# Kernel optimization log

Measured on AMD Instinct MI355X. Metric: run time of the kernel, lower is better.

## Reference

```python
import jax, jax.numpy as jnp
import numpy as np
from jax import lax

B, C, H, W = 2, 256, 128, 128
NC, NP = 80, 9  # num_classes, num_points (3x3 dcn kernel)
PAD = 1


def conv2d(x, w, b=None, pad=1):
    out = lax.conv_general_dilated(x, w, (1, 1), [(pad, pad), (pad, pad)],
                                   dimension_numbers=('NCHW', 'OIHW', 'NCHW'))
    if b is not None:
        out = out + b[None, :, None, None]
    return out


def bilinear_sample(img_bhwc, py, px):
    # zero-padded bilinear sampling; py/px: [B,H,W] float coords
    Hi, Wi = img_bhwc.shape[1], img_bhwc.shape[2]
    y0 = jnp.floor(py)
    x0 = jnp.floor(px)
    wy1 = py - y0
    wx1 = px - x0

    def gather(yc, xc, w):
        valid = (yc >= 0) & (yc <= Hi - 1) & (xc >= 0) & (xc <= Wi - 1)
        yi = jnp.clip(yc, 0, Hi - 1).astype(jnp.int32)
        xi = jnp.clip(xc, 0, Wi - 1).astype(jnp.int32)
        v = jax.vmap(lambda im, yy, xx: im[yy, xx])(img_bhwc, yi, xi)  # [B,H,W,C]
        return v * (w * valid)[..., None]

    return (gather(y0, x0, (1 - wy1) * (1 - wx1)) + gather(y0, x0 + 1, (1 - wy1) * wx1)
            + gather(y0 + 1, x0, wy1 * (1 - wx1)) + gather(y0 + 1, x0 + 1, wy1 * wx1))


def deform_conv(x, offset, weight, mask=None, pad=1):
    # x: [B,C,H,W]; offset: [B,2K,H,W] interleaved (dy,dx) per kernel point;
    # mask: [B,K,H,W] or None (modulated DCN multiplies sampled value by mask as-is)
    kh, kw = weight.shape[2], weight.shape[3]
    xb = jnp.transpose(x, (0, 2, 3, 1))  # [B,H,W,C]
    gy, gx = jnp.meshgrid(jnp.arange(x.shape[2], dtype=x.dtype),
                          jnp.arange(x.shape[3], dtype=x.dtype), indexing='ij')
    acc = 0.
    for k in range(kh * kw):  # fixed structural loop over 9 kernel points
        ky, kx = k // kw, k % kw
        py = gy[None] + (ky - pad) + offset[:, 2 * k]
        px = gx[None] + (kx - pad) + offset[:, 2 * k + 1]
        val = bilinear_sample(xb, py, px)  # [B,H,W,C]
        if mask is not None:
            val = val * mask[:, k][..., None]
        acc = acc + jnp.einsum('bhwc,oc->bohw', val, weight[:, :, ky, kx])
    return acc


def setup_inputs() -> dict:
    key = jax.random.key(0)
    ks = jax.random.split(key, 16)
    d = {"x": jax.random.normal(ks[0], (B, C, H, W), jnp.float32)}

    def w(k, shape):
        return jax.random.normal(k, shape, jnp.float32) * 0.01

    i = 1
    for j in range(3):
        d[f"cls_w{j}"] = w(ks[i], (C, C, 3, 3)); i += 1
        d[f"cls_b{j}"] = jnp.zeros((C,), jnp.float32)
        d[f"reg_w{j}"] = w(ks[i], (C, C, 3, 3)); i += 1
        d[f"reg_b{j}"] = jnp.zeros((C,), jnp.float32)
    d["init_conv_w"] = w(ks[i], (C, C, 3, 3)); i += 1
    d["init_conv_b"] = jnp.zeros((C,), jnp.float32)
    d["init_out_w"] = w(ks[i], (3 * NP, C, 1, 1)); i += 1
    d["init_out_b"] = jnp.zeros((3 * NP,), jnp.float32)
    d["dcn_cls_w"] = w(ks[i], (C, C, 3, 3)); i += 1  # ModulatedDeformConv (bias=False)
    d["cls_out_w"] = w(ks[i], (NC, C, 1, 1)); i += 1
    d["cls_out_b"] = jnp.full((NC,), -4.59511985013459, jnp.float32)  # bias_init_with_prob(0.01)
    d["dcn_ref_w"] = w(ks[i], (C, C, 3, 3)); i += 1  # DeformConv (bias=False)
    d["ref_out_w"] = w(ks[i], (2 * NP, C, 1, 1)); i += 1
    d["ref_out_b"] = jnp.zeros((2 * NP,), jnp.float32)
    return d


def reference(x, cls_w0, cls_b0, reg_w0, reg_b0, cls_w1, cls_b1, reg_w1, reg_b1,
              cls_w2, cls_b2, reg_w2, reg_b2, init_conv_w, init_conv_b,
              init_out_w, init_out_b, dcn_cls_w, cls_out_w, cls_out_b,
              dcn_ref_w, ref_out_w, ref_out_b):
    relu = jax.nn.relu
    cls_feat = x
    for wgt, b in ((cls_w0, cls_b0), (cls_w1, cls_b1), (cls_w2, cls_b2)):
        cls_feat = relu(conv2d(cls_feat, wgt, b, 1))
    pts_feat = x
    for wgt, b in ((reg_w0, reg_b0), (reg_w1, reg_b1), (reg_w2, reg_b2)):
        pts_feat = relu(conv2d(pts_feat, wgt, b, 1))

    pts_out_init = conv2d(relu(conv2d(pts_feat, init_conv_w, init_conv_b, 1)),
                          init_out_w, init_out_b, 0)  # [B,27,H,W]
    o1, o2, mask = (pts_out_init[:, :NP], pts_out_init[:, NP:2 * NP],
                    pts_out_init[:, 2 * NP:])
    offset = jnp.concatenate([o1, o2], axis=1)  # dcn_offset (points_init = 0)

    cls_out = conv2d(relu(deform_conv(cls_feat, offset, dcn_cls_w, mask)),
                     cls_out_w, cls_out_b, 0)
    pts_out_refine = conv2d(relu(deform_conv(pts_feat, offset, dcn_ref_w)),
                            ref_out_w, ref_out_b, 0)
    pts_out_refine = pts_out_refine + lax.stop_gradient(offset)

    # pts2wh_offsets
    pts = pts_out_refine.reshape(B, NP, 2, H, W)
    pts_mean = pts.mean(axis=1, keepdims=True)          # [B,1,2,H,W]
    wh = jnp.abs(pts + pts_mean).max(axis=1)            # [B,2,H,W]
    reg = pts_mean[:, 0]                                # [B,2,H,W]
    return (cls_out, wh, reg)
```

## Files before the change

kernel.cpp:

```cpp
#include <hip/hip_runtime.h>

#define Bn 2
#define Cn 256
#define Hn 128
#define Wn 128
#define HWn 16384
#define NCn 80

typedef __attribute__((ext_vector_type(4))) float f32x4;
typedef __attribute__((ext_vector_type(8))) short bf16x8;

__device__ __forceinline__ float blo(unsigned u) {
    union { unsigned u; float f; } x; x.u = u << 16; return x.f;
}
__device__ __forceinline__ float bhi(unsigned u) {
    union { unsigned u; float f; } x; x.u = u & 0xffff0000u; return x.f;
}
__device__ __forceinline__ unsigned short f2bf(float f) {
    union { float f; unsigned u; } x; x.f = f;
    unsigned u = x.u + 0x7fffu + ((x.u >> 16) & 1u);
    return (unsigned short)(u >> 16);
}

#define GLOAD16(gp, lp) __builtin_amdgcn_global_load_lds( \
    (__attribute__((address_space(1))) unsigned int*)(gp), \
    (__attribute__((address_space(3))) unsigned int*)(lp), 16, 0, 0)

__global__ void zeroK(unsigned short* z) { z[threadIdx.x] = 0; }

__global__ __launch_bounds__(256) void xinK(const float* __restrict__ x,
                                            unsigned short* __restrict__ o) {
    __shared__ float tb[32][33];
    const int b = blockIdx.z;
    const int hw0 = blockIdx.x * 32, c0 = blockIdx.y * 32;
    const int tx = threadIdx.x & 31, ty = threadIdx.x >> 5;
    const float* ip = x + ((size_t)(b * Cn + c0)) * HWn + hw0;
#pragma unroll
    for (int r = 0; r < 4; ++r) tb[ty + 8 * r][tx] = ip[(size_t)(ty + 8 * r) * HWn + tx];
    __syncthreads();
    unsigned short* op = o + ((size_t)(b * HWn + hw0)) * Cn + c0;
#pragma unroll
    for (int r = 0; r < 4; ++r) op[(size_t)(ty + 8 * r) * Cn + tx] = f2bf(tb[tx][ty + 8 * r]);
}

struct WPtrs { const float* p[9]; };
__global__ __launch_bounds__(256) void repackAll(WPtrs wsrc, unsigned short* __restrict__ dst) {
    const int t = blockIdx.x * 256 + threadIdx.x;
    const int widx = t >> 16;
    const int r = t & 65535;
    const float* s = wsrc.p[widx] + (size_t)r * 9;
    float v[9];
#pragma unroll
    for (int k = 0; k < 9; ++k) v[k] = s[k];
    unsigned short* d = dst + (size_t)widx * 589824 + r;
#pragma unroll
    for (int k = 0; k < 9; ++k) d[(size_t)k * 65536] = f2bf(v[k]);
}

struct HPtrs { const float* w[3]; };
__global__ __launch_bounds__(256) void repackHeads(HPtrs hs, unsigned short* __restrict__ dst) {
    const int t = blockIdx.x * 256 + threadIdx.x;
    const int ic = t & 255, row = t >> 8;
    int which, oc, OC;
    if (row < 32)       { which = 0; oc = row;       OC = 27; }
    else if (row < 128) { which = 1; oc = row - 32;  OC = 80; }
    else                { which = 2; oc = row - 128; OC = 18; }
    dst[t] = (oc < OC) ? f2bf(hs.w[which][(size_t)oc * Cn + ic]) : (unsigned short)0;
}

struct CJobs {
    const unsigned short* feat[2];
    const unsigned short* W[2];
    const float* bias[2];
    unsigned short* out[2];
};
__global__ __launch_bounds__(256, 2) void convGemm(CJobs jobs,
                                                   const unsigned short* __restrict__ zb) {
    const int jz = blockIdx.z;
    const unsigned short* feat = jobs.feat[jz];
    const unsigned short* Wp = jobs.W[jz];
    const float* bias = jobs.bias[jz];
    unsigned short* outp = jobs.out[jz];

    __shared__ __align__(16) unsigned short lA[2][8192];
    __shared__ __align__(16) unsigned short lB[2][8192];
    const int tid = threadIdx.x;
    const int l = tid & 63, w = tid >> 6;
    const int w_oc = w & 1, w_px = w >> 1;
    const int ry = (blockIdx.x & 7) * 32 + (blockIdx.x >> 3);
    const int b = ry >> 7, y = ry & 127;
    const int oc0 = blockIdx.y * 128;
    const int lr = l & 15, lg = l >> 4;

    int rI[4], cI[4], dI[4];
#pragma unroll
    for (int i = 0; i < 4; ++i) {
        int ps = (i * 4 + w) * 64 + l;
        rI[i] = ps >> 3;
        cI[i] = ((ps & 7) ^ (rI[i] & 7)) * 8;
        dI[i] = (i * 4 + w) * 512;
    }

    f32x4 acc[4][4];
#pragma unroll
    for (int i = 0; i < 4; ++i)
#pragma unroll
        for (int j = 0; j < 4; ++j) acc[i][j] = (f32x4){0.f, 0.f, 0.f, 0.f};

    auto stage = [&](int p, int bufIdx) {
        const int k = p >> 2, c0 = (p & 3) * 64;
        const int dy = k / 3 - 1, dx = k % 3 - 1;
        const int yy = y + dy;
        const bool vy = (unsigned)yy < (unsigned)Hn;
        const size_t fbase = ((size_t)(b * Hn + yy)) * Wn;
        const unsigned short* wk = Wp + (size_t)k * 65536 + (size_t)oc0 * Cn + c0;
        unsigned short* la = lA[bufIdx];
        unsigned short* lb = lB[bufIdx];
#pragma unroll
        for (int i = 0; i < 4; ++i)
            GLOAD16(wk + rI[i] * Cn + cI[i], la + dI[i]);
#pragma unroll
        for (int i = 0; i < 4; ++i) {
            const int pxs = rI[i] + dx;
            const unsigned short* g = (vy && (unsigned)pxs < (unsigned)Wn)
                ? feat + ((fbase + pxs) * Cn + c0 + cI[i])
                : zb;
            GLOAD16(g, lb + dI[i]);
        }
    };

    stage(0, 0);
    __syncthreads();

#pragma unroll 1
    for (int p = 0; p < 36; ++p) {
        const int cur = p & 1;
        if (p < 35) stage(p + 1, cur ^ 1);
        const unsigned short* la = lA[cur];
        const unsigned short* lb = lB[cur];
#pragma unroll
        for (int h = 0; h < 2; ++h) {
            const int ch = h * 4 + lg;
            bf16x8 av[4], bv[4];
#pragma unroll
            for (int fm = 0; fm < 4; ++fm) {
                const int row = w_oc * 64 + fm * 16 + lr;
                av[fm] = *(const bf16x8*)&la[row * 64 + ((ch ^ (row & 7)) * 8)];
            }
#pragma unroll
            for (int fn = 0; fn < 4; ++fn) {
                const int row = w_px * 64 + fn * 16 + lr;
                bv[fn] = *(const bf16x8*)&lb[row * 64 + ((ch ^ (row & 7)) * 8)];
            }
#pragma unroll
            for (int fm = 0; fm < 4; ++fm)
#pragma unroll
                for (int fn = 0; fn < 4; ++fn)
                    acc[fm][fn] = __builtin_amdgcn_mfma_f32_16x16x32_bf16(
                        av[fm], bv[fn], acc[fm][fn], 0, 0, 0);
        }
        __syncthreads();
    }

#pragma unroll
    for (int fm = 0; fm < 4; ++fm) {
        const int ocb = oc0 + w_oc * 64 + fm * 16 + lg * 4;
        const float b0 = bias[ocb], b1 = bias[ocb + 1], b2 = bias[ocb + 2], b3 = bias[ocb + 3];
#pragma unroll
        for (int fn = 0; fn < 4; ++fn) {
            const int px = w_px * 64 + fn * 16 + lr;
            f32x4 v = acc[fm][fn];
            unsigned u0 = (unsigned)f2bf(fmaxf(v[0] + b0, 0.f)) | ((unsigned)f2bf(fmaxf(v[1] + b1, 0.f)) << 16);
            unsigned u1 = (unsigned)f2bf(fmaxf(v[2] + b2, 0.f)) | ((unsigned)f2bf(fmaxf(v[3] + b3, 0.f)) << 16);
            uint2 st; st.x = u0; st.y = u1;
            *(uint2*)&outp[((size_t)ry * Wn + px) * Cn + ocb] = st;
        }
    }
}

template <bool HASMASK>
__global__ __launch_bounds__(512, 4) void dcnGemm(const unsigned short* __restrict__ feat,
                                                  const float* __restrict__ o27,
                                                  const unsigned short* __restrict__ Wp,
                                                  unsigned short* __restrict__ out) {
    __shared__ __align__(16) unsigned short lA[2][16384];
    __shared__ __align__(16) unsigned short lB[2][4096];
    const int tid = threadIdx.x;
    const int l = tid & 63, w = tid >> 6;
    const int w_oc = w & 3, w_px = w >> 2;
    const int g = (blockIdx.x & 7) * 64 + (blockIdx.x >> 3);
    const int ry = g >> 1, st = g & 1;
    const int b = ry >> 7, y = ry & 127;
    const int x0 = st * 64;
    const int lr = l & 15, lg = l >> 4;

    int rIA[4], cIA[4], dIA[4];
#pragma unroll
    for (int i = 0; i < 4; ++i) {
        int ps = (i * 8 + w) * 64 + l;
        rIA[i] = ps >> 3;
        cIA[i] = ((ps & 7) ^ (rIA[i] & 7)) * 8;
        dIA[i] = (i * 8 + w) * 512;
    }

    const int sp = tid >> 3;
    const int pc = tid & 7;
    const int xg = x0 + sp;
    const int wslot = sp * 64 + ((pc ^ (sp & 7)) * 8);

    const float* ob = o27 + (size_t)b * 27 * HWn + y * Wn + xg;
    const unsigned short* fb = feat + (size_t)b * HWn * Cn;

    f32x4 acc[4][2];
#pragma unroll
    for (int i = 0; i < 4; ++i)
#pragma unroll
        for (int j = 0; j < 2; ++j) acc[i][j] = (f32x4){0.f, 0.f, 0.f, 0.f};

    int ci0, ci1, ci2, ci3;
    float cw0, cw1, cw2, cw3;

    auto sampParams = [&](int k) {
        const float offy = ob[(size_t)(2 * k) * HWn];
        const float offx = ob[(size_t)(2 * k + 1) * HWn];
        const float m = HASMASK ? ob[(size_t)(18 + k) * HWn] : 1.f;
        const float py = (float)(y + k / 3 - 1) + offy;
        const float px = (float)(xg + k % 3 - 1) + offx;
        const float y0f = floorf(py), x0f = floorf(px);
        const float wy1 = py - y0f, wx1 = px - x0f;
        const int iy0 = (int)y0f, ix0 = (int)x0f;
        const int iy1 = iy0 + 1, ix1 = ix0 + 1;
        const bool vy0 = (unsigned)iy0 < (unsigned)Hn, vy1 = (unsigned)iy1 < (unsigned)Hn;
        const bool vx0 = (unsigned)ix0 < (unsigned)Wn, vx1 = (unsigned)ix1 < (unsigned)Wn;
        const int yc0 = min(max(iy0, 0), Hn - 1), yc1 = min(max(iy1, 0), Hn - 1);
        const int xc0 = min(max(ix0, 0), Wn - 1), xc1 = min(max(ix1, 0), Wn - 1);
        cw0 = (vy0 && vx0) ? (1.f - wy1) * (1.f - wx1) * m : 0.f;
        cw1 = (vy0 && vx1) ? (1.f - wy1) * wx1 * m : 0.f;
        cw2 = (vy1 && vx0) ? wy1 * (1.f - wx1) * m : 0.f;
        cw3 = (vy1 && vx1) ? wy1 * wx1 * m : 0.f;
        ci0 = (yc0 * Wn + xc0) * Cn;
        ci1 = (yc0 * Wn + xc1) * Cn;
        ci2 = (yc1 * Wn + xc0) * Cn;
        ci3 = (yc1 * Wn + xc1) * Cn;
    };

    int4 q0, q1, q2, q3;
    auto cornerLoads = [&](int p) {
        const int cb = (p & 3) * 64 + pc * 8;
        q0 = *(const int4*)(fb + ci0 + cb);
        q1 = *(const int4*)(fb + ci1 + cb);
        q2 = *(const int4*)(fb + ci2 + cb);
        q3 = *(const int4*)(fb + ci3 + cb);
    };
    auto stageA = [&](int p, int bufIdx) {
        const int k = p >> 2, c0 = (p & 3) * 64;
        const unsigned short* wk = Wp + (size_t)k * 65536 + c0;
        unsigned short* la = lA[bufIdx];
#pragma unroll
        for (int i = 0; i < 4; ++i)
            GLOAD16(wk + rIA[i] * Cn + cIA[i], la + dIA[i]);
    };
    auto interpWrite = [&](int bufIdx) {
        unsigned u[4];
#pragma unroll
        for (int jj = 0; jj < 4; ++jj) {
            const unsigned a0 = ((const unsigned*)&q0)[jj];
            const unsigned a1 = ((const unsigned*)&q1)[jj];
            const unsigned a2 = ((const unsigned*)&q2)[jj];
            const unsigned a3 = ((const unsigned*)&q3)[jj];
            float e0 = cw0 * blo(a0) + cw1 * blo(a1) + cw2 * blo(a2) + cw3 * blo(a3);
            float e1 = cw0 * bhi(a0) + cw1 * bhi(a1) + cw2 * bhi(a2) + cw3 * bhi(a3);
            u[jj] = (unsigned)f2bf(e0) | ((unsigned)f2bf(e1) << 16);
        }
        int4 pk; pk.x = u[0]; pk.y = u[1]; pk.z = u[2]; pk.w = u[3];
        *(int4*)&lB[bufIdx][wslot] = pk;
    };

    sampParams(0);
    stageA(0, 0);
    cornerLoads(0);
    interpWrite(0);
    __syncthreads();

#pragma unroll 1
    for (int p = 0; p < 36; ++p) {
        const int cur = p & 1;
        if (p < 35) {
            if (((p + 1) & 3) == 0) sampParams((p + 1) >> 2);
            stageA(p + 1, cur ^ 1);
            cornerLoads(p + 1);
        }
        const unsigned short* la = lA[cur];
        const unsigned short* lb = lB[cur];
#pragma unroll
        for (int h = 0; h < 2; ++h) {
            const int ch = h * 4 + lg;
            bf16x8 av[4], bv[2];
#pragma unroll
            for (int fm = 0; fm < 4; ++fm) {
                const int row = w_oc * 64 + fm * 16 + lr;
                av[fm] = *(const bf16x8*)&la[row * 64 + ((ch ^ (row & 7)) * 8)];
            }
#pragma unroll
            for (int fn = 0; fn < 2; ++fn) {
                const int row = w_px * 32 + fn * 16 + lr;
                bv[fn] = *(const bf16x8*)&lb[row * 64 + ((ch ^ (row & 7)) * 8)];
            }
#pragma unroll
            for (int fm = 0; fm < 4; ++fm)
#pragma unroll
                for (int fn = 0; fn < 2; ++fn)
                    acc[fm][fn] = __builtin_amdgcn_mfma_f32_16x16x32_bf16(
                        av[fm], bv[fn], acc[fm][fn], 0, 0, 0);
        }
        if (p < 35) interpWrite(cur ^ 1);
        __syncthreads();
    }

#pragma unroll
    for (int fm = 0; fm < 4; ++fm) {
        const int ocb = w_oc * 64 + fm * 16 + lg * 4;
#pragma unroll
        for (int fn = 0; fn < 2; ++fn) {
            const int px = x0 + w_px * 32 + fn * 16 + lr;
            f32x4 v = acc[fm][fn];
            unsigned u0 = (unsigned)f2bf(fmaxf(v[0], 0.f)) | ((unsigned)f2bf(fmaxf(v[1], 0.f)) << 16);
            unsigned u1 = (unsigned)f2bf(fmaxf(v[2], 0.f)) | ((unsigned)f2bf(fmaxf(v[3], 0.f)) << 16);
            uint2 stv; stv.x = u0; stv.y = u1;
            *(uint2*)&out[((size_t)ry * Wn + px) * Cn + ocb] = stv;
        }
    }
}

template <int OC, int PM, bool ADD, bool POST>
__global__ __launch_bounds__(256, 2) void headGemm(const unsigned short* __restrict__ feat,
                                                   const unsigned short* __restrict__ Wp,
                                                   const float* __restrict__ bias,
                                                   float* __restrict__ out,
                                                   const float* __restrict__ add,
                                                   int addC,
                                                   float* __restrict__ reg) {
    constexpr int MF = PM / 16;
    constexpr int NA = PM * 8 / 256;
    __shared__ __align__(16) unsigned short lA[PM * 64];
    __shared__ __align__(16) unsigned short lB[128 * 64];
    __shared__ float lR[POST ? 18 : 1][POST ? 128 : 1];
    const int tid = threadIdx.x;
    const int l = tid & 63, w = tid >> 6;
    const int ry = (blockIdx.x & 7) * 32 + (blockIdx.x >> 3);
    const int b = ry >> 7, y = ry & 127;
    const int lr = l & 15, lg = l >> 4;

    int rIA[NA], cIA[NA], dIA[NA];
#pragma unroll
    for (int i = 0; i < NA; ++i) {
        int ps = (i * 4 + w) * 64 + l;
        rIA[i] = ps >> 3;
        cIA[i] = ((ps & 7) ^ (rIA[i] & 7)) * 8;
        dIA[i] = (i * 4 + w) * 512;
    }
    int rIB[4], cIB[4], dIB[4];
#pragma unroll
    for (int i = 0; i < 4; ++i) {
        int ps = (i * 4 + w) * 64 + l;
        rIB[i] = ps >> 3;
        cIB[i] = ((ps & 7) ^ (rIB[i] & 7)) * 8;
        dIB[i] = (i * 4 + w) * 512;
    }

    f32x4 acc[MF][2];
#pragma unroll
    for (int i = 0; i < MF; ++i)
#pragma unroll
        for (int j = 0; j < 2; ++j) acc[i][j] = (f32x4){0.f, 0.f, 0.f, 0.f};

    const unsigned short* frow = feat + ((size_t)ry * Wn) * Cn;

#pragma unroll 1
    for (int cc = 0; cc < 4; ++cc) {
        const int c0 = cc * 64;
#pragma unroll
        for (int i = 0; i < NA; ++i)
            GLOAD16(Wp + (size_t)rIA[i] * Cn + c0 + cIA[i], &lA[dIA[i]]);
#pragma unroll
        for (int i = 0; i < 4; ++i)
            GLOAD16(frow + (size_t)rIB[i] * Cn + c0 + cIB[i], &lB[dIB[i]]);
        __syncthreads();
#pragma unroll
        for (int h = 0; h < 2; ++h) {
            const int ch = h * 4 + lg;
            bf16x8 av[MF], bv[2];
#pragma unroll
            for (int fm = 0; fm < MF; ++fm) {
                const int row = fm * 16 + lr;
                av[fm] = *(const bf16x8*)&lA[row * 64 + ((ch ^ (row & 7)) * 8)];
            }
#pragma unroll
            for (int fn = 0; fn < 2; ++fn) {
                const int row = w * 32 + fn * 16 + lr;
                bv[fn] = *(const bf16x8*)&lB[row * 64 + ((ch ^ (row & 7)) * 8)];
            }
#pragma unroll
            for (int fm = 0; fm < MF; ++fm)
#pragma unroll
                for (int fn = 0; fn < 2; ++fn)
                    acc[fm][fn] = __builtin_amdgcn_mfma_f32_16x16x32_bf16(
                        av[fm], bv[fn], acc[fm][fn], 0, 0, 0);
        }
        __syncthreads();
    }

    if (!POST) {
#pragma unroll
        for (int fm = 0; fm < MF; ++fm) {
            const int ocb = fm * 16 + lg * 4;
            if (ocb >= OC) break;
#pragma unroll
            for (int j = 0; j < 4; ++j) {
                const int oc = ocb + j;
                if (oc >= OC) break;
                const float bs = bias[oc];
#pragma unroll
                for (int fn = 0; fn < 2; ++fn) {
                    const int px = w * 32 + fn * 16 + lr;
                    float r = acc[fm][fn][j] + bs;
                    if (ADD) r += add[((size_t)(b * addC + oc)) * HWn + y * Wn + px];
                    out[((size_t)(b * OC + oc)) * HWn + y * Wn + px] = r;
                }
            }
        }
    } else {
#pragma unroll
        for (int fm = 0; fm < MF; ++fm) {
            const int ocb = fm * 16 + lg * 4;
#pragma unroll
            for (int j = 0; j < 4; ++j) {
                const int oc = ocb + j;
                if (oc < 18) {
                    const float bs = bias[oc];
#pragma unroll
                    for (int fn = 0; fn < 2; ++fn) {
                        const int px = w * 32 + fn * 16 + lr;
                        float r = acc[fm][fn][j] + bs
                                + add[((size_t)(b * addC + oc)) * HWn + y * Wn + px];
                        lR[oc][px] = r;
                    }
                }
            }
        }
        __syncthreads();
        if (tid < 128) {
            const int px = tid;
            float v[18];
#pragma unroll
            for (int c = 0; c < 18; ++c) v[c] = lR[c][px];
            float s0 = 0.f, s1 = 0.f;
#pragma unroll
            for (int q = 0; q < 9; ++q) { s0 += v[2 * q]; s1 += v[2 * q + 1]; }
            float m0 = s0 * (1.f / 9.f), m1 = s1 * (1.f / 9.f);
            float w0 = 0.f, w1 = 0.f;
#pragma unroll
            for (int q = 0; q < 9; ++q) {
                w0 = fmaxf(w0, fabsf(v[2 * q] + m0));
                w1 = fmaxf(w1, fabsf(v[2 * q + 1] + m1));
            }
            const size_t hw = (size_t)y * Wn + px;
            out[(size_t)(b * 2 + 0) * HWn + hw] = w0;
            out[(size_t)(b * 2 + 1) * HWn + hw] = w1;
            reg[(size_t)(b * 2 + 0) * HWn + hw] = m0;
            reg[(size_t)(b * 2 + 1) * HWn + hw] = m1;
        }
    }
}

extern "C" void kernel_launch(void* const* d_in, const int* in_sizes, int n_in,
                              void* d_out, int out_size, void* d_ws, size_t ws_size,
                              hipStream_t stream) {
    const float* x           = (const float*)d_in[0];
    const float* cls_w0      = (const float*)d_in[1];
    const float* cls_b0      = (const float*)d_in[2];
    const float* reg_w0      = (const float*)d_in[3];
    const float* reg_b0      = (const float*)d_in[4];
    const float* cls_w1      = (const float*)d_in[5];
    const float* cls_b1      = (const float*)d_in[6];
    const float* reg_w1      = (const float*)d_in[7];
    const float* reg_b1      = (const float*)d_in[8];
    const float* cls_w2      = (const float*)d_in[9];
    const float* cls_b2      = (const float*)d_in[10];
    const float* reg_w2      = (const float*)d_in[11];
    const float* reg_b2      = (const float*)d_in[12];
    const float* init_conv_w = (const float*)d_in[13];
    const float* init_conv_b = (const float*)d_in[14];
    const float* init_out_w  = (const float*)d_in[15];
    const float* init_out_b  = (const float*)d_in[16];
    const float* dcn_cls_w   = (const float*)d_in[17];
    const float* cls_out_w   = (const float*)d_in[18];
    const float* cls_out_b   = (const float*)d_in[19];
    const float* dcn_ref_w   = (const float*)d_in[20];
    const float* ref_out_w   = (const float*)d_in[21];
    const float* ref_out_b   = (const float*)d_in[22];

    float* out = (float*)d_out;

    char* ws = (char*)d_ws;
    const size_t IMG = (size_t)Bn * HWn * Cn * sizeof(unsigned short);
    unsigned short* B0 = (unsigned short*)ws; ws += IMG;
    unsigned short* B1 = (unsigned short*)ws; ws += IMG;
    unsigned short* B2 = (unsigned short*)ws; ws += IMG;
    unsigned short* B3 = (unsigned short*)ws; ws += IMG;
    float* O27 = (float*)ws; ws += (size_t)Bn * 27 * HWn * sizeof(float);
    const size_t WSZ = (size_t)9 * Cn * Cn;
    unsigned short* Wpk = (unsigned short*)ws; ws += 9 * WSZ * sizeof(unsigned short);
    unsigned short* WhAll = (unsigned short*)ws; ws += 160 * Cn * sizeof(unsigned short);
    unsigned short* ZB = (unsigned short*)ws;  ws += 512;

    unsigned short* W_cls0 = Wpk + 0 * WSZ;
    unsigned short* W_cls1 = Wpk + 1 * WSZ;
    unsigned short* W_cls2 = Wpk + 2 * WSZ;
    unsigned short* W_reg0 = Wpk + 3 * WSZ;
    unsigned short* W_reg1 = Wpk + 4 * WSZ;
    unsigned short* W_reg2 = Wpk + 5 * WSZ;
    unsigned short* W_init = Wpk + 6 * WSZ;
    unsigned short* W_dcls = Wpk + 7 * WSZ;
    unsigned short* W_dref = Wpk + 8 * WSZ;
    unsigned short* Wh27 = WhAll;
    unsigned short* Wh80 = WhAll + 32 * Cn;
    unsigned short* Wh18 = WhAll + 128 * Cn;

    const dim3 blk(256);
    const dim3 xgrd(512, 8, Bn);

    zeroK<<<1, 128, 0, stream>>>(ZB);
    WPtrs wp;
    wp.p[0] = cls_w0; wp.p[1] = cls_w1; wp.p[2] = cls_w2;
    wp.p[3] = reg_w0; wp.p[4] = reg_w1; wp.p[5] = reg_w2;
    wp.p[6] = init_conv_w; wp.p[7] = dcn_cls_w; wp.p[8] = dcn_ref_w;
    repackAll<<<2304, blk, 0, stream>>>(wp, Wpk);
    HPtrs hp; hp.w[0] = init_out_w; hp.w[1] = cls_out_w; hp.w[2] = ref_out_w;
    repackHeads<<<160, blk, 0, stream>>>(hp, WhAll);
    xinK<<<xgrd, blk, 0, stream>>>(x, B0);

    CJobs j;
    j.feat[0] = B0; j.W[0] = W_cls0; j.bias[0] = cls_b0; j.out[0] = B1;
    j.feat[1] = B0; j.W[1] = W_reg0; j.bias[1] = reg_b0; j.out[1] = B2;
    convGemm<<<dim3(256, 2, 2), blk, 0, stream>>>(j, ZB);
    j.feat[0] = B1; j.W[0] = W_cls1; j.bias[0] = cls_b1; j.out[0] = B3;
    j.feat[1] = B2; j.W[1] = W_reg1; j.bias[1] = reg_b1; j.out[1] = B0;
    convGemm<<<dim3(256, 2, 2), blk, 0, stream>>>(j, ZB);
    j.feat[0] = B3; j.W[0] = W_cls2; j.bias[0] = cls_b2; j.out[0] = B1;
    j.feat[1] = B0; j.W[1] = W_reg2; j.bias[1] = reg_b2; j.out[1] = B2;
    convGemm<<<dim3(256, 2, 2), blk, 0, stream>>>(j, ZB);
    j.feat[0] = B2; j.W[0] = W_init; j.bias[0] = init_conv_b; j.out[0] = B3;
    j.feat[1] = B2; j.W[1] = W_init; j.bias[1] = init_conv_b; j.out[1] = B3;
    convGemm<<<dim3(256, 2, 1), blk, 0, stream>>>(j, ZB);
    headGemm<27, 32, false, false><<<256, blk, 0, stream>>>(B3, Wh27, init_out_b, O27, nullptr, 0, nullptr);
    dcnGemm<true><<<512, dim3(512), 0, stream>>>(B1, O27, W_dcls, B0);
    headGemm<80, 96, false, false><<<256, blk, 0, stream>>>(B0, Wh80, cls_out_b, out, nullptr, 0, nullptr);
    dcnGemm<false><<<512, dim3(512), 0, stream>>>(B2, O27, W_dref, B3);
    headGemm<18, 32, true, true><<<256, blk, 0, stream>>>(
        B3, Wh18, ref_out_b,
        out + (size_t)Bn * NCn * HWn,
        O27, 27,
        out + (size_t)Bn * NCn * HWn + (size_t)Bn * 2 * HWn);
}
```

Before: 584.3 us.

## Merge launches, batch both DCN passes, prefetch offsets, use packed bf16 convert

Merges zero-fill and both weight repacks into one kernel. Runs the two deformable convolutions as one 1024-block launch, and the two tail head GEMMs as one launch. Inside the DCN kernel, offset/mask loads are prefetched a sampling step ahead and corner loads are issued before the A-tile staging. Float-to-bf16 packing switches to the hardware v_cvt_pk_bf16_f32 instruction. The mask flag becomes a runtime branch instead of a template parameter, and the packed convert may round differently from the software version.

```diff
diff --git a/kernel.cpp b/kernel.cpp
--- a/kernel.cpp
+++ b/kernel.cpp
@@ -13,20 +13,23 @@
 __device__ __forceinline__ float blo(unsigned u) {
     union { unsigned u; float f; } x; x.u = u << 16; return x.f;
 }
-__device__ __forceinline__ float bhi(unsigned u) {
-    union { unsigned u; float f; } x; x.u = u & 0xffff0000u; return x.f;
+__device__ __forceinline__ float braw(unsigned u) {
+    union { unsigned u; float f; } x; x.u = u; return x.f;
 }
 __device__ __forceinline__ unsigned short f2bf(float f) {
     union { float f; unsigned u; } x; x.f = f;
     unsigned u = x.u + 0x7fffu + ((x.u >> 16) & 1u);
     return (unsigned short)(u >> 16);
 }
+__device__ __forceinline__ unsigned pk2bf(float e0, float e1) {
+    unsigned r;
+    asm("v_cvt_pk_bf16_f32 %0, %1, %2" : "=v"(r) : "v"(e0), "v"(e1));
+    return r;
+}
 
 #define GLOAD16(gp, lp) __builtin_amdgcn_global_load_lds( \
     (__attribute__((address_space(1))) unsigned int*)(gp), \
     (__attribute__((address_space(3))) unsigned int*)(lp), 16, 0, 0)
-
-__global__ void zeroK(unsigned short* z) { z[threadIdx.x] = 0; }
 
 __global__ __launch_bounds__(256) void xinK(const float* __restrict__ x,
                                             unsigned short* __restrict__ o) {
@@ -43,29 +46,32 @@
     for (int r = 0; r < 4; ++r) op[(size_t)(ty + 8 * r) * Cn + tx] = f2bf(tb[tx][ty + 8 * r]);
 }
 
-struct WPtrs { const float* p[9]; };
-__global__ __launch_bounds__(256) void repackAll(WPtrs wsrc, unsigned short* __restrict__ dst) {
-    const int t = blockIdx.x * 256 + threadIdx.x;
-    const int widx = t >> 16;
-    const int r = t & 65535;
-    const float* s = wsrc.p[widx] + (size_t)r * 9;
-    float v[9];
-#pragma unroll
-    for (int k = 0; k < 9; ++k) v[k] = s[k];
-    unsigned short* d = dst + (size_t)widx * 589824 + r;
-#pragma unroll
-    for (int k = 0; k < 9; ++k) d[(size_t)k * 65536] = f2bf(v[k]);
-}
-
-struct HPtrs { const float* w[3]; };
-__global__ __launch_bounds__(256) void repackHeads(HPtrs hs, unsigned short* __restrict__ dst) {
-    const int t = blockIdx.x * 256 + threadIdx.x;
-    const int ic = t & 255, row = t >> 8;
-    int which, oc, OC;
-    if (row < 32)       { which = 0; oc = row;       OC = 27; }
-    else if (row < 128) { which = 1; oc = row - 32;  OC = 80; }
-    else                { which = 2; oc = row - 128; OC = 18; }
-    dst[t] = (oc < OC) ? f2bf(hs.w[which][(size_t)oc * Cn + ic]) : (unsigned short)0;
+struct RPtrs { const float* w3[9]; const float* wh[3]; };
+__global__ __launch_bounds__(256) void repackAllK(RPtrs rp,
+                                                  unsigned short* __restrict__ dst3,
+                                                  unsigned short* __restrict__ dstH,
+                                                  unsigned short* __restrict__ zb) {
+    if (blockIdx.x < 2304) {
+        if (blockIdx.x == 0) { zb[threadIdx.x] = 0; zb[256 + threadIdx.x] = 0; }
+        const int t = blockIdx.x * 256 + threadIdx.x;
+        const int widx = t >> 16;
+        const int r = t & 65535;
+        const float* s = rp.w3[widx] + (size_t)r * 9;
+        float v[9];
+#pragma unroll
+        for (int k = 0; k < 9; ++k) v[k] = s[k];
+        unsigned short* d = dst3 + (size_t)widx * 589824 + r;
+#pragma unroll
+        for (int k = 0; k < 9; ++k) d[(size_t)k * 65536] = f2bf(v[k]);
+    } else {
+        const int t = (blockIdx.x - 2304) * 256 + threadIdx.x;
+        const int ic = t & 255, row = t >> 8;
+        int which, oc, OC;
+        if (row < 32)       { which = 0; oc = row;       OC = 27; }
+        else if (row < 128) { which = 1; oc = row - 32;  OC = 80; }
+        else                { which = 2; oc = row - 128; OC = 18; }
+        dstH[t] = (oc < OC) ? f2bf(rp.wh[which][(size_t)oc * Cn + ic]) : (unsigned short)0;
+    }
 }
 
 struct CJobs {
@@ -170,25 +176,35 @@
         for (int fn = 0; fn < 4; ++fn) {
             const int px = w_px * 64 + fn * 16 + lr;
             f32x4 v = acc[fm][fn];
-            unsigned u0 = (unsigned)f2bf(fmaxf(v[0] + b0, 0.f)) | ((unsigned)f2bf(fmaxf(v[1] + b1, 0.f)) << 16);
-            unsigned u1 = (unsigned)f2bf(fmaxf(v[2] + b2, 0.f)) | ((unsigned)f2bf(fmaxf(v[3] + b3, 0.f)) << 16);
-            uint2 st; st.x = u0; st.y = u1;
+            uint2 st;
+            st.x = pk2bf(fmaxf(v[0] + b0, 0.f), fmaxf(v[1] + b1, 0.f));
+            st.y = pk2bf(fmaxf(v[2] + b2, 0.f), fmaxf(v[3] + b3, 0.f));
             *(uint2*)&outp[((size_t)ry * Wn + px) * Cn + ocb] = st;
         }
     }
 }
 
-template <bool HASMASK>
-__global__ __launch_bounds__(512, 4) void dcnGemm(const unsigned short* __restrict__ feat,
-                                                  const float* __restrict__ o27,
-                                                  const unsigned short* __restrict__ Wp,
-                                                  unsigned short* __restrict__ out) {
+struct DJobs {
+    const unsigned short* feat[2];
+    const unsigned short* W[2];
+    unsigned short* out[2];
+    int mask[2];
+};
+__global__ __launch_bounds__(512, 4) void dcnGemm(DJobs jobs,
+                                                  const float* __restrict__ o27) {
+    const int jz = blockIdx.x >> 9;
+    const unsigned short* feat = jobs.feat[jz];
+    const unsigned short* Wp = jobs.W[jz];
+    unsigned short* outp = jobs.out[jz];
+    const bool HASMASK = jobs.mask[jz] != 0;
+
     __shared__ __align__(16) unsigned short lA[2][16384];
     __shared__ __align__(16) unsigned short lB[2][4096];
     const int tid = threadIdx.x;
     const int l = tid & 63, w = tid >> 6;
     const int w_oc = w & 3, w_px = w >> 2;
-    const int g = (blockIdx.x & 7) * 64 + (blockIdx.x >> 3);
+    const int lb_ = blockIdx.x & 511;
+    const int g = (lb_ & 7) * 64 + (lb_ >> 3);
     const int ry = g >> 1, st = g & 1;
     const int b = ry >> 7, y = ry & 127;
     const int x0 = st * 64;
@@ -219,13 +235,11 @@
 
     int ci0, ci1, ci2, ci3;
     float cw0, cw1, cw2, cw3;
-
-    auto sampParams = [&](int k) {
-        const float offy = ob[(size_t)(2 * k) * HWn];
-        const float offx = ob[(size_t)(2 * k + 1) * HWn];
-        const float m = HASMASK ? ob[(size_t)(18 + k) * HWn] : 1.f;
-        const float py = (float)(y + k / 3 - 1) + offy;
-        const float px = (float)(xg + k % 3 - 1) + offx;
+    float pofy, pofx, pom;
+
+    auto sampFromRegs = [&](int k) {
+        const float py = (float)(y + k / 3 - 1) + pofy;
+        const float px = (float)(xg + k % 3 - 1) + pofx;
         const float y0f = floorf(py), x0f = floorf(px);
         const float wy1 = py - y0f, wx1 = px - x0f;
         const int iy0 = (int)y0f, ix0 = (int)x0f;
@@ -234,14 +248,19 @@
         const bool vx0 = (unsigned)ix0 < (unsigned)Wn, vx1 = (unsigned)ix1 < (unsigned)Wn;
         const int yc0 = min(max(iy0, 0), Hn - 1), yc1 = min(max(iy1, 0), Hn - 1);
         const int xc0 = min(max(ix0, 0), Wn - 1), xc1 = min(max(ix1, 0), Wn - 1);
-        cw0 = (vy0 && vx0) ? (1.f - wy1) * (1.f - wx1) * m : 0.f;
-        cw1 = (vy0 && vx1) ? (1.f - wy1) * wx1 * m : 0.f;
-        cw2 = (vy1 && vx0) ? wy1 * (1.f - wx1) * m : 0.f;
-        cw3 = (vy1 && vx1) ? wy1 * wx1 * m : 0.f;
+        cw0 = (vy0 && vx0) ? (1.f - wy1) * (1.f - wx1) * pom : 0.f;
+        cw1 = (vy0 && vx1) ? (1.f - wy1) * wx1 * pom : 0.f;
+        cw2 = (vy1 && vx0) ? wy1 * (1.f - wx1) * pom : 0.f;
+        cw3 = (vy1 && vx1) ? wy1 * wx1 * pom : 0.f;
         ci0 = (yc0 * Wn + xc0) * Cn;
         ci1 = (yc0 * Wn + xc1) * Cn;
         ci2 = (yc1 * Wn + xc0) * Cn;
         ci3 = (yc1 * Wn + xc1) * Cn;
+    };
+    auto prefOff = [&](int k) {
+        pofy = ob[(size_t)(2 * k) * HWn];
+        pofx = ob[(size_t)(2 * k + 1) * HWn];
+        pom = HASMASK ? ob[(size_t)(18 + k) * HWn] : 1.f;
     };
 
     int4 q0, q1, q2, q3;
@@ -261,7 +280,7 @@
             GLOAD16(wk + rIA[i] * Cn + cIA[i], la + dIA[i]);
     };
     auto interpWrite = [&](int bufIdx) {
-        unsigned u[4];
+        unsigned uu[4];
 #pragma unroll
         for (int jj = 0; jj < 4; ++jj) {
             const unsigned a0 = ((const unsigned*)&q0)[jj];
@@ -269,26 +288,29 @@
             const unsigned a2 = ((const unsigned*)&q2)[jj];
             const unsigned a3 = ((const unsigned*)&q3)[jj];
             float e0 = cw0 * blo(a0) + cw1 * blo(a1) + cw2 * blo(a2) + cw3 * blo(a3);
-            float e1 = cw0 * bhi(a0) + cw1 * bhi(a1) + cw2 * bhi(a2) + cw3 * bhi(a3);
-            u[jj] = (unsigned)f2bf(e0) | ((unsigned)f2bf(e1) << 16);
-        }
-        int4 pk; pk.x = u[0]; pk.y = u[1]; pk.z = u[2]; pk.w = u[3];
+            float e1 = cw0 * braw(a0) + cw1 * braw(a1) + cw2 * braw(a2) + cw3 * braw(a3);
+            uu[jj] = pk2bf(e0, e1);
+        }
+        int4 pk; pk.x = uu[0]; pk.y = uu[1]; pk.z = uu[2]; pk.w = uu[3];
         *(int4*)&lB[bufIdx][wslot] = pk;
     };
 
-    sampParams(0);
+    prefOff(0);
+    sampFromRegs(0);
+    cornerLoads(0);
     stageA(0, 0);
-    cornerLoads(0);
     interpWrite(0);
+    prefOff(1);
     __syncthreads();
 
 #pragma unroll 1
     for (int p = 0; p < 36; ++p) {
         const int cur = p & 1;
         if (p < 35) {
-            if (((p + 1) & 3) == 0) sampParams((p + 1) >> 2);
+            if (((p + 1) & 3) == 0) sampFromRegs((p + 1) >> 2);
+            cornerLoads(p + 1);
             stageA(p + 1, cur ^ 1);
-            cornerLoads(p + 1);
+            if ((p & 3) == 1 && (p >> 2) < 8) prefOff((p >> 2) + 2);
         }
         const unsigned short* la = lA[cur];
         const unsigned short* lb = lB[cur];
@@ -319,35 +341,35 @@
 
 #pragma unroll
     for (int fm = 0; fm < 4; ++fm) {
-        const int ocb = w_oc * 64 + fm * 16 + lg * 4;
+        const int oc = w_oc * 64 + fm * 16 + lg * 4;
 #pragma unroll
         for (int fn = 0; fn < 2; ++fn) {
             const int px = x0 + w_px * 32 + fn * 16 + lr;
             f32x4 v = acc[fm][fn];
-            unsigned u0 = (unsigned)f2bf(fmaxf(v[0], 0.f)) | ((unsigned)f2bf(fmaxf(v[1], 0.f)) << 16);
-            unsigned u1 = (unsigned)f2bf(fmaxf(v[2], 0.f)) | ((unsigned)f2bf(fmaxf(v[3], 0.f)) << 16);
-            uint2 stv; stv.x = u0; stv.y = u1;
-            *(uint2*)&out[((size_t)ry * Wn + px) * Cn + ocb] = stv;
-        }
-    }
-}
+            uint2 stv;
+            stv.x = pk2bf(fmaxf(v[0], 0.f), fmaxf(v[1], 0.f));
+            stv.y = pk2bf(fmaxf(v[2], 0.f), fmaxf(v[3], 0.f));
+            *(uint2*)&outp[((size_t)ry * Wn + px) * Cn + oc] = stv;
+        }
+    }
+}
+
 
 template <int OC, int PM, bool ADD, bool POST>
-__global__ __launch_bounds__(256, 2) void headGemm(const unsigned short* __restrict__ feat,
-                                                   const unsigned short* __restrict__ Wp,
-                                                   const float* __restrict__ bias,
-                                                   float* __restrict__ out,
-                                                   const float* __restrict__ add,
-                                                   int addC,
-                                                   float* __restrict__ reg) {
+__device__ __forceinline__ void headBody(int bx,
+                                         const unsigned short* __restrict__ feat,
+                                         const unsigned short* __restrict__ Wp,
+                                         const float* __restrict__ bias,
+                                         float* __restrict__ out,
+                                         const float* __restrict__ add, int addC,
+                                         float* __restrict__ reg,
+                                         unsigned short* lA, unsigned short* lB,
+                                         float (*lR)[128]) {
     constexpr int MF = PM / 16;
     constexpr int NA = PM * 8 / 256;
-    __shared__ __align__(16) unsigned short lA[PM * 64];
-    __shared__ __align__(16) unsigned short lB[128 * 64];
-    __shared__ float lR[POST ? 18 : 1][POST ? 128 : 1];
     const int tid = threadIdx.x;
     const int l = tid & 63, w = tid >> 6;
-    const int ry = (blockIdx.x & 7) * 32 + (blockIdx.x >> 3);
+    const int ry = (bx & 7) * 32 + (bx >> 3);
     const int b = ry >> 7, y = ry & 127;
     const int lr = l & 15, lg = l >> 4;
 
@@ -470,6 +492,38 @@
             reg[(size_t)(b * 2 + 0) * HWn + hw] = m0;
             reg[(size_t)(b * 2 + 1) * HWn + hw] = m1;
         }
+    }
+}
+
+__global__ __launch_bounds__(256, 2) void head27K(const unsigned short* __restrict__ feat,
+                                                  const unsigned short* __restrict__ Wp,
+                                                  const float* __restrict__ bias,
+                                                  float* __restrict__ out) {
+    __shared__ __align__(16) unsigned short sA[32 * 64];
+    __shared__ __align__(16) unsigned short sB[128 * 64];
+    headBody<27, 32, false, false>(blockIdx.x, feat, Wp, bias, out,
+                                   nullptr, 0, nullptr, sA, sB, nullptr);
+}
+
+__global__ __launch_bounds__(256, 2) void headTailK(const unsigned short* __restrict__ f80,
+                                                    const unsigned short* __restrict__ W80,
+                                                    const float* __restrict__ b80,
+                                                    float* __restrict__ out80,
+                                                    const unsigned short* __restrict__ f18,
+                                                    const unsigned short* __restrict__ W18,
+                                                    const float* __restrict__ b18,
+                                                    const float* __restrict__ add27,
+                                                    float* __restrict__ wh,
+                                                    float* __restrict__ reg) {
+    __shared__ __align__(16) unsigned short sA[96 * 64];
+    __shared__ __align__(16) unsigned short sB[128 * 64];
+    __shared__ float sR[18][128];
+    if (blockIdx.x < 256) {
+        headBody<80, 96, false, false>(blockIdx.x, f80, W80, b80, out80,
+                                       nullptr, 0, nullptr, sA, sB, nullptr);
+    } else {
+        headBody<18, 32, true, true>(blockIdx.x - 256, f18, W18, b18, wh,
+                                     add27, 27, reg, sA, sB, sR);
     }
 }
 
@@ -512,7 +566,7 @@
     const size_t WSZ = (size_t)9 * Cn * Cn;
     unsigned short* Wpk = (unsigned short*)ws; ws += 9 * WSZ * sizeof(unsigned short);
     unsigned short* WhAll = (unsigned short*)ws; ws += 160 * Cn * sizeof(unsigned short);
-    unsigned short* ZB = (unsigned short*)ws;  ws += 512;
+    unsigned short* ZB = (unsigned short*)ws;  ws += 1024;
 
     unsigned short* W_cls0 = Wpk + 0 * WSZ;
     unsigned short* W_cls1 = Wpk + 1 * WSZ;
@@ -530,14 +584,12 @@
     const dim3 blk(256);
     const dim3 xgrd(512, 8, Bn);
 
-    zeroK<<<1, 128, 0, stream>>>(ZB);
-    WPtrs wp;
-    wp.p[0] = cls_w0; wp.p[1] = cls_w1; wp.p[2] = cls_w2;
-    wp.p[3] = reg_w0; wp.p[4] = reg_w1; wp.p[5] = reg_w2;
-    wp.p[6] = init_conv_w; wp.p[7] = dcn_cls_w; wp.p[8] = dcn_ref_w;
-    repackAll<<<2304, blk, 0, stream>>>(wp, Wpk);
-    HPtrs hp; hp.w[0] = init_out_w; hp.w[1] = cls_out_w; hp.w[2] = ref_out_w;
-    repackHeads<<<160, blk, 0, stream>>>(hp, WhAll);
+    RPtrs rp;
+    rp.w3[0] = cls_w0; rp.w3[1] = cls_w1; rp.w3[2] = cls_w2;
+    rp.w3[3] = reg_w0; rp.w3[4] = reg_w1; rp.w3[5] = reg_w2;
+    rp.w3[6] = init_conv_w; rp.w3[7] = dcn_cls_w; rp.w3[8] = dcn_ref_w;
+    rp.wh[0] = init_out_w; rp.wh[1] = cls_out_w; rp.wh[2] = ref_out_w;
+    repackAllK<<<2464, blk, 0, stream>>>(rp, Wpk, WhAll, ZB);
     xinK<<<xgrd, blk, 0, stream>>>(x, B0);
 
     CJobs j;
@@ -551,15 +603,15 @@
     j.feat[1] = B0; j.W[1] = W_reg2; j.bias[1] = reg_b2; j.out[1] = B2;
     convGemm<<<dim3(256, 2, 2), blk, 0, stream>>>(j, ZB);
     j.feat[0] = B2; j.W[0] = W_init; j.bias[0] = init_conv_b; j.out[0] = B3;
-    j.feat[1] = B2; j.W[1] = W_init; j.bias[1] = init_conv_b; j.out[1] = B3;
     convGemm<<<dim3(256, 2, 1), blk, 0, stream>>>(j, ZB);
-    headGemm<27, 32, false, false><<<256, blk, 0, stream>>>(B3, Wh27, init_out_b, O27, nullptr, 0, nullptr);
-    dcnGemm<true><<<512, dim3(512), 0, stream>>>(B1, O27, W_dcls, B0);
-    headGemm<80, 96, false, false><<<256, blk, 0, stream>>>(B0, Wh80, cls_out_b, out, nullptr, 0, nullptr);
-    dcnGemm<false><<<512, dim3(512), 0, stream>>>(B2, O27, W_dref, B3);
-    headGemm<18, 32, true, true><<<256, blk, 0, stream>>>(
-        B3, Wh18, ref_out_b,
+    head27K<<<256, blk, 0, stream>>>(B3, Wh27, init_out_b, O27);
+    DJobs dj;
+    dj.feat[0] = B1; dj.W[0] = W_dcls; dj.out[0] = B0; dj.mask[0] = 1;
+    dj.feat[1] = B2; dj.W[1] = W_dref; dj.out[1] = B3; dj.mask[1] = 0;
+    dcnGemm<<<1024, dim3(512), 0, stream>>>(dj, O27);
+    headTailK<<<512, blk, 0, stream>>>(
+        B0, Wh80, cls_out_b, out,
+        B3, Wh18, ref_out_b, O27,
         out + (size_t)Bn * NCn * HWn,
-        O27, 27,
         out + (size_t)Bn * NCn * HWn + (size_t)Bn * 2 * HWn);
 }
```

Measured after the change: 567.8 us. 1.03x faster.
